# Performance work log

Hardware: AMD Instinct MI355X
Metric: run time of the kernel (lower is better)

## Reference

```python
import jax, jax.numpy as jnp
import numpy as np

EPS = 1e-5  # BatchNorm eps


def _add_self_loops(edge_index, num_nodes):
    loop = jnp.arange(num_nodes, dtype=edge_index.dtype)
    src = jnp.concatenate([edge_index[0], loop])
    dst = jnp.concatenate([edge_index[1], loop])
    return src, dst


def _gcn_conv(x, src, dst, norm, W, b, num_nodes):
    # PyG GCNConv: out = D^{-1/2} (A+I) D^{-1/2} (x W) + b
    h = x @ W                                # [N, out_dim]
    msg = h[src] * norm[:, None]             # [E+N, out_dim] gathered messages
    out = jax.ops.segment_sum(msg, dst, num_segments=num_nodes)
    return out + b


def _batch_norm(x, gamma, beta):
    # training-mode batch statistics over the node dimension (biased var)
    mean = jnp.mean(x, axis=0)
    var = jnp.var(x, axis=0)
    return (x - mean) * jax.lax.rsqrt(var + EPS) * gamma + beta


def setup_inputs() -> dict:
    key = jax.random.key(0)
    ks = jax.random.split(key, 10)
    N, E = 50000, 800000
    d_in, d_h, d_mid, d_out = 1536, 512, 128, 5

    x = jax.random.normal(ks[0], (N, d_in), dtype=jnp.float32)
    edge_index = jax.random.randint(ks[1], (2, E), 0, N, dtype=jnp.int32)

    def glorot(k, fan_in, fan_out):
        s = jnp.sqrt(6.0 / (fan_in + fan_out))
        return jax.random.uniform(k, (fan_in, fan_out), jnp.float32, -s, s)

    return {
        "x": x,
        "edge_index": edge_index,
        "W1": glorot(ks[2], d_in, d_h), "b1": jnp.zeros((d_h,), jnp.float32),
        "W2": glorot(ks[3], d_h, d_mid), "b2": jnp.zeros((d_mid,), jnp.float32),
        "W3": glorot(ks[4], d_mid, d_out), "b3": jnp.zeros((d_out,), jnp.float32),
        "gamma1": jnp.ones((d_h,), jnp.float32), "beta1": jnp.zeros((d_h,), jnp.float32),
        "gamma2": jnp.ones((d_mid,), jnp.float32), "beta2": jnp.zeros((d_mid,), jnp.float32),
    }


def reference(x, edge_index, W1, b1, W2, b2, W3, b3, gamma1, beta1, gamma2, beta2):
    N = x.shape[0]
    src, dst = _add_self_loops(edge_index, N)
    # symmetric degree normalization deg^{-1/2}[src] * deg^{-1/2}[dst]
    deg = jax.ops.segment_sum(jnp.ones_like(dst, dtype=x.dtype), dst, num_segments=N)
    inv_sqrt = jnp.where(deg > 0, jax.lax.rsqrt(deg), 0.0)
    norm = inv_sqrt[src] * inv_sqrt[dst]

    h = _gcn_conv(x, src, dst, norm, W1, b1, N)
    h = jax.nn.relu(_batch_norm(h, gamma1, beta1))  # dropout is identity in eval
    h = _gcn_conv(h, src, dst, norm, W2, b2, N)
    h = jax.nn.relu(_batch_norm(h, gamma2, beta2))
    h = _gcn_conv(h, src, dst, norm, W3, b3, N)
    return jax.nn.log_softmax(h, axis=1)
```

## Files before the change

kernel.cpp:

```cpp
#include <hip/hip_runtime.h>
#include <cstddef>
#include <cstdint>

typedef short s16x8 __attribute__((ext_vector_type(8)));
typedef unsigned short u16x4 __attribute__((ext_vector_type(4)));
typedef unsigned short u16x8 __attribute__((ext_vector_type(8)));
typedef float f32x4 __attribute__((ext_vector_type(4)));

__device__ __forceinline__ unsigned short f2bf(float f) {
  unsigned int u = __float_as_uint(f);
  u = (u + 0x7fffu + ((u >> 16) & 1u)) >> 16;
  return (unsigned short)u;
}
__device__ __forceinline__ float bf2f(unsigned short u) {
  return __uint_as_float(((unsigned int)u) << 16);
}

__device__ __forceinline__ void gl2lds16(const unsigned short* g, unsigned short* l) {
  __builtin_amdgcn_global_load_lds(
      (const __attribute__((address_space(1))) unsigned int*)g,
      (__attribute__((address_space(3))) unsigned int*)l, 16, 0, 0);
}
__device__ __forceinline__ void gl2lds16f(const float* g, float* l) {
  __builtin_amdgcn_global_load_lds(
      (const __attribute__((address_space(1))) unsigned int*)g,
      (__attribute__((address_space(3))) unsigned int*)l, 16, 0, 0);
}

static inline size_t alignup(size_t x) { return (x + 255) & ~(size_t)255; }

__global__ void count_kernel(const int* __restrict__ dst, int* __restrict__ counts, int E) {
  int e = blockIdx.x * blockDim.x + threadIdx.x;
  if (e < E) atomicAdd(&counts[dst[e]], 1);
}

__global__ void block_sum_kernel(const int* __restrict__ counts, int* __restrict__ bsum, int n) {
  __shared__ int red[256];
  int i = blockIdx.x * 256 + threadIdx.x;
  red[threadIdx.x] = (i < n) ? counts[i] : 0;
  __syncthreads();
  #pragma unroll
  for (int o = 128; o > 0; o >>= 1) {
    if (threadIdx.x < o) red[threadIdx.x] += red[threadIdx.x + o];
    __syncthreads();
  }
  if (threadIdx.x == 0) bsum[blockIdx.x] = red[0];
}

__global__ void scan_bsum_kernel(int* __restrict__ bsum, int nb) {
  __shared__ int s[256];
  int t = threadIdx.x;
  s[t] = (t < nb) ? bsum[t] : 0;
  __syncthreads();
  #pragma unroll
  for (int o = 1; o < 256; o <<= 1) {
    int v = (t >= o) ? s[t - o] : 0;
    __syncthreads();
    s[t] += v;
    __syncthreads();
  }
  if (t < nb) bsum[t] = (t == 0) ? 0 : s[t - 1];
}

__global__ void scan_apply_kernel(const int* __restrict__ counts, const int* __restrict__ bpre,
                                  int* __restrict__ offsets, float* __restrict__ inv_s, int n) {
  __shared__ int s[256];
  int t = threadIdx.x;
  int i = blockIdx.x * 256 + t;
  int c = (i < n) ? counts[i] : 0;
  s[t] = c;
  __syncthreads();
  #pragma unroll
  for (int o = 1; o < 256; o <<= 1) {
    int v = (t >= o) ? s[t - o] : 0;
    __syncthreads();
    s[t] += v;
    __syncthreads();
  }
  if (i < n) {
    offsets[i + 1] = s[t] + bpre[blockIdx.x];
    inv_s[i] = rsqrtf((float)(c + 1));
  }
  if (i == 0) offsets[0] = 0;
}

__global__ void fill_kernel(const int* __restrict__ src, const int* __restrict__ dst,
                            const int* __restrict__ offsets, int* __restrict__ cursor,
                            int* __restrict__ csr_src, int E) {
  int e = blockIdx.x * blockDim.x + threadIdx.x;
  if (e >= E) return;
  int d = dst[e];
  int pos = atomicAdd(&cursor[d], 1);
  csr_src[offsets[d] + pos] = src[e];
}

__global__ void transpose_both_kernel(const float* __restrict__ W1, unsigned short* __restrict__ W1t,
                                      const float* __restrict__ W2, unsigned short* __restrict__ W2t) {
  __shared__ float tile[32][33];
  int b = blockIdx.x;
  const float* W;
  unsigned short* Wt;
  int K, N, kx, ny;
  if (b < 768) { W = W1; Wt = W1t; K = 1536; N = 512; kx = b % 48; ny = b / 48; }
  else { b -= 768; W = W2; Wt = W2t; K = 512; N = 128; kx = b % 16; ny = b / 16; }
  int k0 = kx * 32, n0 = ny * 32;
  int tx = threadIdx.x & 31, ty = threadIdx.x >> 5;
  #pragma unroll
  for (int i = 0; i < 32; i += 8)
    tile[ty + i][tx] = W[(size_t)(k0 + ty + i) * N + n0 + tx];
  __syncthreads();
  #pragma unroll
  for (int i = 0; i < 32; i += 8)
    Wt[(size_t)(n0 + ty + i) * K + k0 + tx] = f2bf(tile[tx][ty + i]);
}

__global__ __launch_bounds__(512) void gemm1_kernel(
    const float* __restrict__ A, const unsigned short* __restrict__ B,
    unsigned short* __restrict__ C, int M) {
  __shared__ __align__(16) float As[2][128 * 32];
  __shared__ __align__(16) unsigned short Bs[2][256 * 32];
  const int K = 1536;
  const int NT = 48;
  int tid = threadIdx.x, lane = tid & 63, w = tid >> 6;

  int nwg = gridDim.x * gridDim.y;
  int orig = blockIdx.y * gridDim.x + blockIdx.x;
  int q = nwg >> 3, r = nwg & 7;
  int xcd = orig & 7, loc = orig >> 3;
  int wg = (xcd < r) ? xcd * (q + 1) + loc : r * (q + 1) + (xcd - r) * q + loc;
  int bx = wg & 1, by = wg >> 1;

  int m0 = by * 128, n0 = bx * 256;
  int wm = (w >> 2) * 64, wn = (w & 3) * 64;

  f32x4 acc[4][4];
  #pragma unroll
  for (int i = 0; i < 4; i++)
    #pragma unroll
    for (int j = 0; j < 4; j++) acc[i][j] = (f32x4){0.f, 0.f, 0.f, 0.f};

  int row0 = tid >> 3, slot0 = tid & 7;
  int row1 = 64 + row0;
  const float* agp0 = &A[(size_t)min(m0 + row0, M - 1) * K + ((slot0 ^ (row0 & 7)) << 2)];
  const float* agp1 = &A[(size_t)min(m0 + row1, M - 1) * K + ((slot0 ^ (row1 & 7)) << 2)];
  int adst0 = tid * 4, adst1 = (512 + tid) * 4;
  int brow = tid >> 2, bslot = tid & 3;
  int bsrc = (bslot ^ ((brow >> 1) & 3)) << 3;
  const unsigned short* bgp0 = &B[(size_t)(n0 + brow) * K + bsrc];
  const unsigned short* bgp1 = &B[(size_t)(n0 + 128 + brow) * K + bsrc];
  int bdst0 = tid * 8, bdst1 = (512 + tid) * 8;

  gl2lds16f(agp0, &As[0][adst0]);
  gl2lds16f(agp1, &As[0][adst1]);
  gl2lds16(bgp0, &Bs[0][bdst0]);
  gl2lds16(bgp1, &Bs[0][bdst1]);
  __syncthreads();

  int cur = 0;
  for (int t = 0; t < NT; t++) {
    if (t + 1 < NT) {
      int kb = (t + 1) * 32;
      gl2lds16f(agp0 + kb, &As[cur ^ 1][adst0]);
      gl2lds16f(agp1 + kb, &As[cur ^ 1][adst1]);
      gl2lds16(bgp0 + kb, &Bs[cur ^ 1][bdst0]);
      gl2lds16(bgp1 + kb, &Bs[cur ^ 1][bdst1]);
    }
    int jc = lane >> 4;
    s16x8 af[4], bfr[4];
    #pragma unroll
    for (int i = 0; i < 4; i++) {
      int rr = wm + i * 16 + (lane & 15);
      f32x4 v0 = *reinterpret_cast<const f32x4*>(&As[cur][rr * 32 + (((2 * jc) ^ (rr & 7)) << 2)]);
      f32x4 v1 = *reinterpret_cast<const f32x4*>(&As[cur][rr * 32 + (((2 * jc + 1) ^ (rr & 7)) << 2)]);
      unsigned int c0, c1, c2, c3;
      asm("v_cvt_pk_bf16_f32 %0, %1, %2" : "=v"(c0) : "v"(v0[0]), "v"(v0[1]));
      asm("v_cvt_pk_bf16_f32 %0, %1, %2" : "=v"(c1) : "v"(v0[2]), "v"(v0[3]));
      asm("v_cvt_pk_bf16_f32 %0, %1, %2" : "=v"(c2) : "v"(v1[0]), "v"(v1[1]));
      asm("v_cvt_pk_bf16_f32 %0, %1, %2" : "=v"(c3) : "v"(v1[2]), "v"(v1[3]));
      uint4 pk;
      pk.x = c0; pk.y = c1; pk.z = c2; pk.w = c3;
      af[i] = __builtin_bit_cast(s16x8, pk);
      int rn = wn + i * 16 + (lane & 15);
      bfr[i] = *reinterpret_cast<const s16x8*>(
          &Bs[cur][rn * 32 + ((jc ^ ((rn >> 1) & 3)) << 3)]);
    }
    #pragma unroll
    for (int i = 0; i < 4; i++)
      #pragma unroll
      for (int j = 0; j < 4; j++)
        acc[i][j] = __builtin_amdgcn_mfma_f32_16x16x32_bf16(af[i], bfr[j], acc[i][j], 0, 0, 0);
    __syncthreads();
    cur ^= 1;
  }

  #pragma unroll
  for (int i = 0; i < 4; i++) {
    #pragma unroll
    for (int j = 0; j < 4; j++) {
      int col = n0 + wn + j * 16 + (lane & 15);
      #pragma unroll
      for (int r2 = 0; r2 < 4; r2++) {
        int row = m0 + wm + i * 16 + (lane >> 4) * 4 + r2;
        if (row < M) C[(size_t)row * 512 + col] = f2bf(acc[i][j][r2]);
      }
    }
  }
}

#define LDT 72
__global__ __launch_bounds__(256) void gemm2_kernel(
    const unsigned short* __restrict__ A, const unsigned short* __restrict__ Bt,
    const float* __restrict__ accum, const float* __restrict__ gamma,
    const float* __restrict__ beta, unsigned short* __restrict__ C, int M, float invN) {
  const int N = 128, K = 512;
  __shared__ unsigned short As[64 * LDT];
  __shared__ unsigned short Bs[128 * LDT];
  __shared__ float scs[512], shs[512];
  int tid = threadIdx.x;
  int m0 = blockIdx.y * 64;
  int w = tid >> 6, lane = tid & 63;
  int wm = (w >> 1) * 32, wn = (w & 1) * 64;

  for (int c = tid; c < 512; c += 256) {
    float mean = accum[c] * invN;
    float var = accum[512 + c] * invN - mean * mean;
    float s = gamma[c] * rsqrtf(var + 1e-5f);
    scs[c] = s;
    shs[c] = beta[c] - mean * s;
  }
  __syncthreads();

  f32x4 acc[2][4];
  #pragma unroll
  for (int i = 0; i < 2; i++)
    #pragma unroll
    for (int j = 0; j < 4; j++) acc[i][j] = (f32x4){0.f, 0.f, 0.f, 0.f};

  for (int k0 = 0; k0 < K; k0 += 64) {
    #pragma unroll
    for (int r = 0; r < 2; r++) {
      int idx = r * 256 + tid;
      int row = idx >> 3;
      int seg = (idx & 7) * 8;
      int gr = m0 + row;
      u16x8 v = (u16x8){0, 0, 0, 0, 0, 0, 0, 0};
      if (gr < M) v = *reinterpret_cast<const u16x8*>(&A[(size_t)gr * K + k0 + seg]);
      int c = k0 + seg;
      u16x8 p;
      #pragma unroll
      for (int j = 0; j < 8; j++) {
        float f = fmaxf(bf2f(v[j]) * scs[c + j] + shs[c + j], 0.f);
        p[j] = f2bf(f);
      }
      *reinterpret_cast<u16x8*>(&As[row * LDT + seg]) = p;
    }
    #pragma unroll
    for (int r = 0; r < 4; r++) {
      int idx = r * 256 + tid;
      int n = idx >> 3;
      int seg = (idx & 7) * 8;
      u16x8 v = *reinterpret_cast<const u16x8*>(&Bt[(size_t)n * K + k0 + seg]);
      *reinterpret_cast<u16x8*>(&Bs[n * LDT + seg]) = v;
    }
    __syncthreads();
    #pragma unroll
    for (int ks = 0; ks < 2; ks++) {
      s16x8 af[2], bfr[4];
      #pragma unroll
      for (int i = 0; i < 2; i++)
        af[i] = *reinterpret_cast<const s16x8*>(
            &As[(wm + i * 16 + (lane & 15)) * LDT + ks * 32 + (lane >> 4) * 8]);
      #pragma unroll
      for (int j = 0; j < 4; j++)
        bfr[j] = *reinterpret_cast<const s16x8*>(
            &Bs[(wn + j * 16 + (lane & 15)) * LDT + ks * 32 + (lane >> 4) * 8]);
      #pragma unroll
      for (int i = 0; i < 2; i++)
        #pragma unroll
        for (int j = 0; j < 4; j++)
          acc[i][j] = __builtin_amdgcn_mfma_f32_16x16x32_bf16(af[i], bfr[j], acc[i][j], 0, 0, 0);
    }
    __syncthreads();
  }
  #pragma unroll
  for (int i = 0; i < 2; i++) {
    #pragma unroll
    for (int j = 0; j < 4; j++) {
      int col = wn + j * 16 + (lane & 15);
      #pragma unroll
      for (int r = 0; r < 4; r++) {
        int row = m0 + wm + i * 16 + (lane >> 4) * 4 + r;
        if (row < M) C[(size_t)row * N + col] = f2bf(acc[i][j][r]);
      }
    }
  }
}

__global__ void agg512_kernel(const unsigned short* __restrict__ h, const int* __restrict__ offsets,
                              const int* __restrict__ csr, const float* __restrict__ inv_s,
                              unsigned short* __restrict__ out, int n) {
  int wv = threadIdx.x >> 6, lane = threadIdx.x & 63;
  int node = blockIdx.x * 4 + wv;
  if (node >= n) return;
  const u16x8* h8 = reinterpret_cast<const u16x8*>(h);
  float di = inv_s[node];
  size_t rb = (size_t)node * 64;
  float acc[8];
  u16x8 v0 = h8[rb + lane];
  float dd = di * di;
  #pragma unroll
  for (int j = 0; j < 8; j++) acc[j] = bf2f(v0[j]) * dd;
  int e = offsets[node], e1 = offsets[node + 1];
  for (; e + 3 < e1; e += 4) {
    int sA = csr[e], sB = csr[e + 1], sC = csr[e + 2], sD = csr[e + 3];
    float wA = inv_s[sA] * di, wB = inv_s[sB] * di;
    float wC = inv_s[sC] * di, wD = inv_s[sD] * di;
    u16x8 vA = h8[(size_t)sA * 64 + lane];
    u16x8 vB = h8[(size_t)sB * 64 + lane];
    u16x8 vC = h8[(size_t)sC * 64 + lane];
    u16x8 vD = h8[(size_t)sD * 64 + lane];
    #pragma unroll
    for (int j = 0; j < 8; j++)
      acc[j] += (bf2f(vA[j]) * wA + bf2f(vB[j]) * wB) +
                (bf2f(vC[j]) * wC + bf2f(vD[j]) * wD);
  }
  for (; e < e1; e++) {
    int sA = csr[e];
    float wA = inv_s[sA] * di;
    u16x8 vA = h8[(size_t)sA * 64 + lane];
    #pragma unroll
    for (int j = 0; j < 8; j++) acc[j] += bf2f(vA[j]) * wA;
  }
  u16x8 o;
  #pragma unroll
  for (int j = 0; j < 8; j++) o[j] = f2bf(acc[j]);
  reinterpret_cast<u16x8*>(out)[rb + lane] = o;
}

__global__ void agg128_kernel(const unsigned short* __restrict__ h, const int* __restrict__ offsets,
                              const int* __restrict__ csr, const float* __restrict__ inv_s,
                              unsigned short* __restrict__ out, int n) {
  int wv = threadIdx.x >> 6, lane = threadIdx.x & 63;
  int node = blockIdx.x * 4 + wv;
  if (node >= n) return;
  const unsigned int* h2 = reinterpret_cast<const unsigned int*>(h);
  float di = inv_s[node];
  size_t rb = (size_t)node * 64;
  unsigned int u0 = h2[rb + lane];
  float dd = di * di;
  float alo = __uint_as_float(u0 << 16) * dd;
  float ahi = __uint_as_float(u0 & 0xffff0000u) * dd;
  int e = offsets[node], e1 = offsets[node + 1];
  for (; e + 3 < e1; e += 4) {
    int sA = csr[e], sB = csr[e + 1], sC = csr[e + 2], sD = csr[e + 3];
    float wA = inv_s[sA] * di, wB = inv_s[sB] * di;
    float wC = inv_s[sC] * di, wD = inv_s[sD] * di;
    unsigned int uA = h2[(size_t)sA * 64 + lane];
    unsigned int uB = h2[(size_t)sB * 64 + lane];
    unsigned int uC = h2[(size_t)sC * 64 + lane];
    unsigned int uD = h2[(size_t)sD * 64 + lane];
    alo += (__uint_as_float(uA << 16) * wA + __uint_as_float(uB << 16) * wB) +
           (__uint_as_float(uC << 16) * wC + __uint_as_float(uD << 16) * wD);
    ahi += (__uint_as_float(uA & 0xffff0000u) * wA + __uint_as_float(uB & 0xffff0000u) * wB) +
           (__uint_as_float(uC & 0xffff0000u) * wC + __uint_as_float(uD & 0xffff0000u) * wD);
  }
  for (; e < e1; e++) {
    int sA = csr[e];
    float wA = inv_s[sA] * di;
    unsigned int uA = h2[(size_t)sA * 64 + lane];
    alo += __uint_as_float(uA << 16) * wA;
    ahi += __uint_as_float(uA & 0xffff0000u) * wA;
  }
  unsigned int uo = ((unsigned int)f2bf(ahi) << 16) | (unsigned int)f2bf(alo);
  reinterpret_cast<unsigned int*>(out)[rb + lane] = uo;
}

__global__ void bn_stats512_kernel(const unsigned short* __restrict__ x, float* __restrict__ accum,
                                   int nrows, int rpb) {
  int r0 = blockIdx.x * rpb, r1 = min(nrows, r0 + rpb);
  int t = threadIdx.x;
  const unsigned int* x2 = reinterpret_cast<const unsigned int*>(x);
  float s0 = 0.f, q0 = 0.f, s1 = 0.f, q1 = 0.f;
  for (int r = r0; r < r1; r++) {
    unsigned int u = x2[(size_t)r * 256 + t];
    float lo = __uint_as_float(u << 16);
    float hi = __uint_as_float(u & 0xffff0000u);
    s0 += lo; q0 += lo * lo; s1 += hi; q1 += hi * hi;
  }
  atomicAdd(&accum[2 * t], s0);
  atomicAdd(&accum[2 * t + 1], s1);
  atomicAdd(&accum[512 + 2 * t], q0);
  atomicAdd(&accum[512 + 2 * t + 1], q1);
}

__global__ void bn_stats128_kernel(const unsigned short* __restrict__ x, float* __restrict__ accum,
                                   int nrows, int rpb) {
  int r0 = blockIdx.x * rpb, r1 = min(nrows, r0 + rpb);
  int t = threadIdx.x;
  int colu = t & 63, rofs = t >> 6;
  const unsigned int* x2 = reinterpret_cast<const unsigned int*>(x);
  float s0 = 0.f, q0 = 0.f, s1 = 0.f, q1 = 0.f;
  for (int r = r0 + rofs; r < r1; r += 4) {
    unsigned int u = x2[(size_t)r * 64 + colu];
    float lo = __uint_as_float(u << 16);
    float hi = __uint_as_float(u & 0xffff0000u);
    s0 += lo; q0 += lo * lo; s1 += hi; q1 += hi * hi;
  }
  atomicAdd(&accum[2 * colu], s0);
  atomicAdd(&accum[2 * colu + 1], s1);
  atomicAdd(&accum[128 + 2 * colu], q0);
  atomicAdd(&accum[128 + 2 * colu + 1], q1);
}

__global__ void gemm3_kernel(const unsigned short* __restrict__ A, const float* __restrict__ W,
                             const float* __restrict__ accum, const float* __restrict__ gamma,
                             const float* __restrict__ beta, float* __restrict__ C, int M,
                             float invN) {
  __shared__ float Ws[128 * 5];
  __shared__ float scs[128], shs[128];
  int tid = threadIdx.x;
  for (int i = tid; i < 128 * 5; i += blockDim.x) Ws[i] = W[i];
  if (tid < 128) {
    float mean = accum[tid] * invN;
    float var = accum[128 + tid] * invN - mean * mean;
    float s = gamma[tid] * rsqrtf(var + 1e-5f);
    scs[tid] = s;
    shs[tid] = beta[tid] - mean * s;
  }
  __syncthreads();
  int row = blockIdx.x * blockDim.x + tid;
  if (row >= M) return;
  float acc[5] = {0.f, 0.f, 0.f, 0.f, 0.f};
  const u16x8* a8 = reinterpret_cast<const u16x8*>(A + (size_t)row * 128);
  for (int k8 = 0; k8 < 16; k8++) {
    u16x8 v = a8[k8];
    int k = k8 * 8;
    #pragma unroll
    for (int j = 0; j < 8; j++) {
      float f = fmaxf(bf2f(v[j]) * scs[k + j] + shs[k + j], 0.f);
      #pragma unroll
      for (int c = 0; c < 5; c++) acc[c] += f * Ws[(k + j) * 5 + c];
    }
  }
  #pragma unroll
  for (int j = 0; j < 5; j++) C[(size_t)row * 5 + j] = acc[j];
}

__global__ void agg3_lsm_kernel(const float* __restrict__ h, const int* __restrict__ offsets,
                                const int* __restrict__ csr, const float* __restrict__ inv_s,
                                const float* __restrict__ b3, float* __restrict__ out, int n) {
  int node = blockIdx.x * blockDim.x + threadIdx.x;
  if (node >= n) return;
  float di = inv_s[node];
  float acc[5];
  #pragma unroll
  for (int j = 0; j < 5; j++) acc[j] = h[(size_t)node * 5 + j] * di * di;
  int s0 = offsets[node], s1 = offsets[node + 1];
  for (int e = s0; e < s1; e++) {
    int s = csr[e];
    float wgt = inv_s[s] * di;
    #pragma unroll
    for (int j = 0; j < 5; j++) acc[j] += h[(size_t)s * 5 + j] * wgt;
  }
  #pragma unroll
  for (int j = 0; j < 5; j++) acc[j] += b3[j];
  float m = acc[0];
  #pragma unroll
  for (int j = 1; j < 5; j++) m = fmaxf(m, acc[j]);
  float sum = 0.f;
  #pragma unroll
  for (int j = 0; j < 5; j++) sum += expf(acc[j] - m);
  float lse = logf(sum);
  #pragma unroll
  for (int j = 0; j < 5; j++) out[(size_t)node * 5 + j] = acc[j] - m - lse;
}

extern "C" void kernel_launch(void* const* d_in, const int* in_sizes, int n_in,
                              void* d_out, int out_size, void* d_ws, size_t ws_size,
                              hipStream_t stream) {
  const float* x      = (const float*)d_in[0];
  const int*   ei     = (const int*)d_in[1];
  const float* W1     = (const float*)d_in[2];
  const float* b3     = (const float*)d_in[7];
  const float* W2     = (const float*)d_in[4];
  const float* W3     = (const float*)d_in[6];
  const float* gamma1 = (const float*)d_in[8];
  const float* beta1  = (const float*)d_in[9];
  const float* gamma2 = (const float*)d_in[10];
  const float* beta2  = (const float*)d_in[11];

  const int N = in_sizes[0] / 1536;
  const int E = in_sizes[1] / 2;
  const int* src = ei;
  const int* dst = ei + E;

  const int mblocks = (N + 127) / 128;
  const int Mpad = mblocks * 128;
  const int nb = (N + 255) / 256;

  char* ws = (char*)d_ws;
  size_t szRA = alignup((size_t)N * 512 * sizeof(float));
  size_t szXB = alignup((size_t)Mpad * 1536 * sizeof(unsigned short));
  char* RAb = ws;
  char* RBb = ws + szRA;
  char* sp = ws + szRA + szXB;
  char* zbase = sp;
  int* counts    = (int*)sp;          sp += alignup((size_t)N * 4);
  int* cursor    = (int*)sp;          sp += alignup((size_t)N * 4);
  float* accumA  = (float*)sp;        sp += alignup(1024 * 4);
  float* accumB  = (float*)sp;        sp += alignup(256 * 4);
  size_t zspan = (size_t)(sp - zbase);
  int* offsets  = (int*)sp;           sp += alignup((size_t)(N + 1) * 4);
  int* csr_src  = (int*)sp;           sp += alignup((size_t)E * 4);
  float* inv_s  = (float*)sp;         sp += alignup((size_t)N * 4);
  unsigned short* W1t = (unsigned short*)sp; sp += alignup((size_t)512 * 1536 * 2);
  unsigned short* W2t = (unsigned short*)sp; sp += alignup((size_t)128 * 512 * 2);
  int* bsum     = (int*)sp;           sp += alignup(256 * 4);

  unsigned short* H1  = (unsigned short*)RAb;
  unsigned short* G1  = (unsigned short*)RBb;
  unsigned short* H2  = (unsigned short*)RAb;
  unsigned short* G2  = (unsigned short*)RBb;
  float*          H3  = (float*)RAb;

  hipMemsetAsync(zbase, 0, zspan, stream);

  count_kernel<<<(E + 255) / 256, 256, 0, stream>>>(dst, counts, E);
  block_sum_kernel<<<nb, 256, 0, stream>>>(counts, bsum, N);
  scan_bsum_kernel<<<1, 256, 0, stream>>>(bsum, nb);
  scan_apply_kernel<<<nb, 256, 0, stream>>>(counts, bsum, offsets, inv_s, N);
  fill_kernel<<<(E + 255) / 256, 256, 0, stream>>>(src, dst, offsets, cursor, csr_src, E);

  transpose_both_kernel<<<832, 256, 0, stream>>>(W1, W1t, W2, W2t);

  int aggblocks = (N + 3) / 4;
  int rpb = (N + 511) / 512;
  float invN = 1.0f / N;

  gemm1_kernel<<<dim3(2, mblocks), 512, 0, stream>>>(x, W1t, H1, N);
  agg512_kernel<<<aggblocks, 256, 0, stream>>>(H1, offsets, csr_src, inv_s, G1, N);
  bn_stats512_kernel<<<512, 256, 0, stream>>>(G1, accumA, N, rpb);

  gemm2_kernel<<<dim3(1, (N + 63) / 64), 256, 0, stream>>>(G1, W2t, accumA, gamma1, beta1, H2, N,
                                                           invN);
  agg128_kernel<<<aggblocks, 256, 0, stream>>>(H2, offsets, csr_src, inv_s, G2, N);
  bn_stats128_kernel<<<512, 256, 0, stream>>>(G2, accumB, N, rpb);

  gemm3_kernel<<<(N + 255) / 256, 256, 0, stream>>>(G2, W3, accumB, gamma2, beta2, H3, N, invN);
  agg3_lsm_kernel<<<(N + 255) / 256, 256, 0, stream>>>(H3, offsets, csr_src, inv_s, b3,
                                                       (float*)d_out, N);
}
```

Baseline: 637.6 us.

## Triple-buffer A tiles in gemm1 with explicit waitcnt-based pipelining

```diff
diff --git a/kernel.cpp b/kernel.cpp
--- a/kernel.cpp
+++ b/kernel.cpp
@@ -117,10 +117,9 @@
 __global__ __launch_bounds__(512) void gemm1_kernel(
     const float* __restrict__ A, const unsigned short* __restrict__ B,
     unsigned short* __restrict__ C, int M) {
-  __shared__ __align__(16) float As[2][128 * 32];
+  __shared__ __align__(16) float As[3][128 * 32];
   __shared__ __align__(16) unsigned short Bs[2][256 * 32];
   const int K = 1536;
-  const int NT = 48;
   int tid = threadIdx.x, lane = tid & 63, w = tid >> 6;
 
   int nwg = gridDim.x * gridDim.y;
@@ -150,28 +149,22 @@
   const unsigned short* bgp1 = &B[(size_t)(n0 + 128 + brow) * K + bsrc];
   int bdst0 = tid * 8, bdst1 = (512 + tid) * 8;
 
-  gl2lds16f(agp0, &As[0][adst0]);
-  gl2lds16f(agp1, &As[0][adst1]);
-  gl2lds16(bgp0, &Bs[0][bdst0]);
-  gl2lds16(bgp1, &Bs[0][bdst1]);
-  __syncthreads();
-
-  int cur = 0;
-  for (int t = 0; t < NT; t++) {
-    if (t + 1 < NT) {
-      int kb = (t + 1) * 32;
-      gl2lds16f(agp0 + kb, &As[cur ^ 1][adst0]);
-      gl2lds16f(agp1 + kb, &As[cur ^ 1][adst1]);
-      gl2lds16(bgp0 + kb, &Bs[cur ^ 1][bdst0]);
-      gl2lds16(bgp1 + kb, &Bs[cur ^ 1][bdst1]);
-    }
+  auto stageA = [&](int kb, float* AsW) {
+    gl2lds16f(agp0 + kb, AsW + adst0);
+    gl2lds16f(agp1 + kb, AsW + adst1);
+  };
+  auto stageB = [&](int kb, unsigned short* BsW) {
+    gl2lds16(bgp0 + kb, BsW + bdst0);
+    gl2lds16(bgp1 + kb, BsW + bdst1);
+  };
+  auto mfma_phase = [&](const float* AsR, const unsigned short* BsR) {
     int jc = lane >> 4;
     s16x8 af[4], bfr[4];
     #pragma unroll
     for (int i = 0; i < 4; i++) {
       int rr = wm + i * 16 + (lane & 15);
-      f32x4 v0 = *reinterpret_cast<const f32x4*>(&As[cur][rr * 32 + (((2 * jc) ^ (rr & 7)) << 2)]);
-      f32x4 v1 = *reinterpret_cast<const f32x4*>(&As[cur][rr * 32 + (((2 * jc + 1) ^ (rr & 7)) << 2)]);
+      f32x4 v0 = *reinterpret_cast<const f32x4*>(&AsR[rr * 32 + (((2 * jc) ^ (rr & 7)) << 2)]);
+      f32x4 v1 = *reinterpret_cast<const f32x4*>(&AsR[rr * 32 + (((2 * jc + 1) ^ (rr & 7)) << 2)]);
       unsigned int c0, c1, c2, c3;
       asm("v_cvt_pk_bf16_f32 %0, %1, %2" : "=v"(c0) : "v"(v0[0]), "v"(v0[1]));
       asm("v_cvt_pk_bf16_f32 %0, %1, %2" : "=v"(c1) : "v"(v0[2]), "v"(v0[3]));
@@ -182,16 +175,46 @@
       af[i] = __builtin_bit_cast(s16x8, pk);
       int rn = wn + i * 16 + (lane & 15);
       bfr[i] = *reinterpret_cast<const s16x8*>(
-          &Bs[cur][rn * 32 + ((jc ^ ((rn >> 1) & 3)) << 3)]);
+          &BsR[rn * 32 + ((jc ^ ((rn >> 1) & 3)) << 3)]);
     }
     #pragma unroll
     for (int i = 0; i < 4; i++)
       #pragma unroll
       for (int j = 0; j < 4; j++)
         acc[i][j] = __builtin_amdgcn_mfma_f32_16x16x32_bf16(af[i], bfr[j], acc[i][j], 0, 0, 0);
-    __syncthreads();
-    cur ^= 1;
-  }
+  };
+
+  stageA(0, As[0]);
+  stageB(0, Bs[0]);
+  stageA(32, As[1]);
+  asm volatile("s_waitcnt vmcnt(2)" ::: "memory");
+  __builtin_amdgcn_s_barrier();
+
+#define G1BODY(T, A0i, A2i, B0i, B1i)                           \
+  stageB(((T) + 1) * 32, Bs[B1i]);                              \
+  stageA(((T) + 2) * 32, As[A2i]);                              \
+  mfma_phase(As[A0i], Bs[B0i]);                                 \
+  asm volatile("s_waitcnt lgkmcnt(0) vmcnt(2)" ::: "memory");   \
+  __builtin_amdgcn_s_barrier();
+
+  for (int tb = 0; tb < 42; tb += 6) {
+    G1BODY(tb + 0, 0, 2, 0, 1)
+    G1BODY(tb + 1, 1, 0, 1, 0)
+    G1BODY(tb + 2, 2, 1, 0, 1)
+    G1BODY(tb + 3, 0, 2, 1, 0)
+    G1BODY(tb + 4, 1, 0, 0, 1)
+    G1BODY(tb + 5, 2, 1, 1, 0)
+  }
+  G1BODY(42, 0, 2, 0, 1)
+  G1BODY(43, 1, 0, 1, 0)
+  G1BODY(44, 2, 1, 0, 1)
+  G1BODY(45, 0, 2, 1, 0)
+#undef G1BODY
+  stageB(47 * 32, Bs[1]);
+  mfma_phase(As[1], Bs[0]);
+  asm volatile("s_waitcnt lgkmcnt(0) vmcnt(0)" ::: "memory");
+  __builtin_amdgcn_s_barrier();
+  mfma_phase(As[2], Bs[1]);
 
   #pragma unroll
   for (int i = 0; i < 4; i++) {
```

Measured after the change: 674.0 us. 1.06x slower.

## Fuse BatchNorm statistics into GCN aggregation kernels

Applied to the files above, without the earlier changes.

```diff
diff --git a/kernel.cpp b/kernel.cpp
--- a/kernel.cpp
+++ b/kernel.cpp
@@ -298,118 +298,122 @@
 
 __global__ void agg512_kernel(const unsigned short* __restrict__ h, const int* __restrict__ offsets,
                               const int* __restrict__ csr, const float* __restrict__ inv_s,
-                              unsigned short* __restrict__ out, int n) {
+                              unsigned short* __restrict__ out, float* __restrict__ accum, int n) {
+  __shared__ float rs[512], rq[512];
   int wv = threadIdx.x >> 6, lane = threadIdx.x & 63;
-  int node = blockIdx.x * 4 + wv;
-  if (node >= n) return;
+  for (int c = threadIdx.x; c < 512; c += 256) { rs[c] = 0.f; rq[c] = 0.f; }
+  __syncthreads();
   const u16x8* h8 = reinterpret_cast<const u16x8*>(h);
-  float di = inv_s[node];
-  size_t rb = (size_t)node * 64;
-  float acc[8];
-  u16x8 v0 = h8[rb + lane];
-  float dd = di * di;
-  #pragma unroll
-  for (int j = 0; j < 8; j++) acc[j] = bf2f(v0[j]) * dd;
-  int e = offsets[node], e1 = offsets[node + 1];
-  for (; e + 3 < e1; e += 4) {
-    int sA = csr[e], sB = csr[e + 1], sC = csr[e + 2], sD = csr[e + 3];
-    float wA = inv_s[sA] * di, wB = inv_s[sB] * di;
-    float wC = inv_s[sC] * di, wD = inv_s[sD] * di;
-    u16x8 vA = h8[(size_t)sA * 64 + lane];
-    u16x8 vB = h8[(size_t)sB * 64 + lane];
-    u16x8 vC = h8[(size_t)sC * 64 + lane];
-    u16x8 vD = h8[(size_t)sD * 64 + lane];
-    #pragma unroll
-    for (int j = 0; j < 8; j++)
-      acc[j] += (bf2f(vA[j]) * wA + bf2f(vB[j]) * wB) +
-                (bf2f(vC[j]) * wC + bf2f(vD[j]) * wD);
-  }
-  for (; e < e1; e++) {
-    int sA = csr[e];
-    float wA = inv_s[sA] * di;
-    u16x8 vA = h8[(size_t)sA * 64 + lane];
-    #pragma unroll
-    for (int j = 0; j < 8; j++) acc[j] += bf2f(vA[j]) * wA;
-  }
-  u16x8 o;
-  #pragma unroll
-  for (int j = 0; j < 8; j++) o[j] = f2bf(acc[j]);
-  reinterpret_cast<u16x8*>(out)[rb + lane] = o;
+  float s[8], qsum[8];
+  #pragma unroll
+  for (int j = 0; j < 8; j++) { s[j] = 0.f; qsum[j] = 0.f; }
+  for (int i = 0; i < 8; i++) {
+    int node = blockIdx.x * 32 + wv * 8 + i;
+    if (node >= n) break;
+    float di = inv_s[node];
+    size_t rb = (size_t)node * 64;
+    float acc[8];
+    u16x8 v0 = h8[rb + lane];
+    float dd = di * di;
+    #pragma unroll
+    for (int j = 0; j < 8; j++) acc[j] = bf2f(v0[j]) * dd;
+    int e = offsets[node], e1 = offsets[node + 1];
+    for (; e + 3 < e1; e += 4) {
+      int sA = csr[e], sB = csr[e + 1], sC = csr[e + 2], sD = csr[e + 3];
+      float wA = inv_s[sA] * di, wB = inv_s[sB] * di;
+      float wC = inv_s[sC] * di, wD = inv_s[sD] * di;
+      u16x8 vA = h8[(size_t)sA * 64 + lane];
+      u16x8 vB = h8[(size_t)sB * 64 + lane];
+      u16x8 vC = h8[(size_t)sC * 64 + lane];
+      u16x8 vD = h8[(size_t)sD * 64 + lane];
+      #pragma unroll
+      for (int j = 0; j < 8; j++)
+        acc[j] += (bf2f(vA[j]) * wA + bf2f(vB[j]) * wB) +
+                  (bf2f(vC[j]) * wC + bf2f(vD[j]) * wD);
+    }
+    for (; e < e1; e++) {
+      int sA = csr[e];
+      float wA = inv_s[sA] * di;
+      u16x8 vA = h8[(size_t)sA * 64 + lane];
+      #pragma unroll
+      for (int j = 0; j < 8; j++) acc[j] += bf2f(vA[j]) * wA;
+    }
+    u16x8 o;
+    #pragma unroll
+    for (int j = 0; j < 8; j++) {
+      float gv = bf2f(f2bf(acc[j]));
+      o[j] = f2bf(acc[j]);
+      s[j] += gv;
+      qsum[j] += gv * gv;
+    }
+    reinterpret_cast<u16x8*>(out)[rb + lane] = o;
+  }
+  #pragma unroll
+  for (int j = 0; j < 8; j++) {
+    atomicAdd(&rs[lane * 8 + j], s[j]);
+    atomicAdd(&rq[lane * 8 + j], qsum[j]);
+  }
+  __syncthreads();
+  for (int c = threadIdx.x; c < 512; c += 256) {
+    atomicAdd(&accum[c], rs[c]);
+    atomicAdd(&accum[512 + c], rq[c]);
+  }
 }
 
 __global__ void agg128_kernel(const unsigned short* __restrict__ h, const int* __restrict__ offsets,
                               const int* __restrict__ csr, const float* __restrict__ inv_s,
-                              unsigned short* __restrict__ out, int n) {
+                              unsigned short* __restrict__ out, float* __restrict__ accum, int n) {
+  __shared__ float rs[128], rq[128];
   int wv = threadIdx.x >> 6, lane = threadIdx.x & 63;
-  int node = blockIdx.x * 4 + wv;
-  if (node >= n) return;
+  if (threadIdx.x < 128) { rs[threadIdx.x] = 0.f; rq[threadIdx.x] = 0.f; }
+  __syncthreads();
   const unsigned int* h2 = reinterpret_cast<const unsigned int*>(h);
-  float di = inv_s[node];
-  size_t rb = (size_t)node * 64;
-  unsigned int u0 = h2[rb + lane];
-  float dd = di * di;
-  float alo = __uint_as_float(u0 << 16) * dd;
-  float ahi = __uint_as_float(u0 & 0xffff0000u) * dd;
-  int e = offsets[node], e1 = offsets[node + 1];
-  for (; e + 3 < e1; e += 4) {
-    int sA = csr[e], sB = csr[e + 1], sC = csr[e + 2], sD = csr[e + 3];
-    float wA = inv_s[sA] * di, wB = inv_s[sB] * di;
-    float wC = inv_s[sC] * di, wD = inv_s[sD] * di;
-    unsigned int uA = h2[(size_t)sA * 64 + lane];
-    unsigned int uB = h2[(size_t)sB * 64 + lane];
-    unsigned int uC = h2[(size_t)sC * 64 + lane];
-    unsigned int uD = h2[(size_t)sD * 64 + lane];
-    alo += (__uint_as_float(uA << 16) * wA + __uint_as_float(uB << 16) * wB) +
-           (__uint_as_float(uC << 16) * wC + __uint_as_float(uD << 16) * wD);
-    ahi += (__uint_as_float(uA & 0xffff0000u) * wA + __uint_as_float(uB & 0xffff0000u) * wB) +
-           (__uint_as_float(uC & 0xffff0000u) * wC + __uint_as_float(uD & 0xffff0000u) * wD);
-  }
-  for (; e < e1; e++) {
-    int sA = csr[e];
-    float wA = inv_s[sA] * di;
-    unsigned int uA = h2[(size_t)sA * 64 + lane];
-    alo += __uint_as_float(uA << 16) * wA;
-    ahi += __uint_as_float(uA & 0xffff0000u) * wA;
-  }
-  unsigned int uo = ((unsigned int)f2bf(ahi) << 16) | (unsigned int)f2bf(alo);
-  reinterpret_cast<unsigned int*>(out)[rb + lane] = uo;
-}
-
-__global__ void bn_stats512_kernel(const unsigned short* __restrict__ x, float* __restrict__ accum,
-                                   int nrows, int rpb) {
-  int r0 = blockIdx.x * rpb, r1 = min(nrows, r0 + rpb);
-  int t = threadIdx.x;
-  const unsigned int* x2 = reinterpret_cast<const unsigned int*>(x);
   float s0 = 0.f, q0 = 0.f, s1 = 0.f, q1 = 0.f;
-  for (int r = r0; r < r1; r++) {
-    unsigned int u = x2[(size_t)r * 256 + t];
-    float lo = __uint_as_float(u << 16);
-    float hi = __uint_as_float(u & 0xffff0000u);
-    s0 += lo; q0 += lo * lo; s1 += hi; q1 += hi * hi;
-  }
-  atomicAdd(&accum[2 * t], s0);
-  atomicAdd(&accum[2 * t + 1], s1);
-  atomicAdd(&accum[512 + 2 * t], q0);
-  atomicAdd(&accum[512 + 2 * t + 1], q1);
-}
-
-__global__ void bn_stats128_kernel(const unsigned short* __restrict__ x, float* __restrict__ accum,
-                                   int nrows, int rpb) {
-  int r0 = blockIdx.x * rpb, r1 = min(nrows, r0 + rpb);
-  int t = threadIdx.x;
-  int colu = t & 63, rofs = t >> 6;
-  const unsigned int* x2 = reinterpret_cast<const unsigned int*>(x);
-  float s0 = 0.f, q0 = 0.f, s1 = 0.f, q1 = 0.f;
-  for (int r = r0 + rofs; r < r1; r += 4) {
-    unsigned int u = x2[(size_t)r * 64 + colu];
-    float lo = __uint_as_float(u << 16);
-    float hi = __uint_as_float(u & 0xffff0000u);
-    s0 += lo; q0 += lo * lo; s1 += hi; q1 += hi * hi;
-  }
-  atomicAdd(&accum[2 * colu], s0);
-  atomicAdd(&accum[2 * colu + 1], s1);
-  atomicAdd(&accum[128 + 2 * colu], q0);
-  atomicAdd(&accum[128 + 2 * colu + 1], q1);
+  for (int i = 0; i < 8; i++) {
+    int node = blockIdx.x * 32 + wv * 8 + i;
+    if (node >= n) break;
+    float di = inv_s[node];
+    size_t rb = (size_t)node * 64;
+    unsigned int u0 = h2[rb + lane];
+    float dd = di * di;
+    float alo = __uint_as_float(u0 << 16) * dd;
+    float ahi = __uint_as_float(u0 & 0xffff0000u) * dd;
+    int e = offsets[node], e1 = offsets[node + 1];
+    for (; e + 3 < e1; e += 4) {
+      int sA = csr[e], sB = csr[e + 1], sC = csr[e + 2], sD = csr[e + 3];
+      float wA = inv_s[sA] * di, wB = inv_s[sB] * di;
+      float wC = inv_s[sC] * di, wD = inv_s[sD] * di;
+      unsigned int uA = h2[(size_t)sA * 64 + lane];
+      unsigned int uB = h2[(size_t)sB * 64 + lane];
+      unsigned int uC = h2[(size_t)sC * 64 + lane];
+      unsigned int uD = h2[(size_t)sD * 64 + lane];
+      alo += (__uint_as_float(uA << 16) * wA + __uint_as_float(uB << 16) * wB) +
+             (__uint_as_float(uC << 16) * wC + __uint_as_float(uD << 16) * wD);
+      ahi += (__uint_as_float(uA & 0xffff0000u) * wA + __uint_as_float(uB & 0xffff0000u) * wB) +
+             (__uint_as_float(uC & 0xffff0000u) * wC + __uint_as_float(uD & 0xffff0000u) * wD);
+    }
+    for (; e < e1; e++) {
+      int sA = csr[e];
+      float wA = inv_s[sA] * di;
+      unsigned int uA = h2[(size_t)sA * 64 + lane];
+      alo += __uint_as_float(uA << 16) * wA;
+      ahi += __uint_as_float(uA & 0xffff0000u) * wA;
+    }
+    unsigned short blo = f2bf(alo), bhi = f2bf(ahi);
+    unsigned int uo = ((unsigned int)bhi << 16) | (unsigned int)blo;
+    reinterpret_cast<unsigned int*>(out)[rb + lane] = uo;
+    float glo = bf2f(blo), ghi = bf2f(bhi);
+    s0 += glo; q0 += glo * glo; s1 += ghi; q1 += ghi * ghi;
+  }
+  atomicAdd(&rs[2 * lane], s0);
+  atomicAdd(&rq[2 * lane], q0);
+  atomicAdd(&rs[2 * lane + 1], s1);
+  atomicAdd(&rq[2 * lane + 1], q1);
+  __syncthreads();
+  if (threadIdx.x < 128) {
+    atomicAdd(&accum[threadIdx.x], rs[threadIdx.x]);
+    atomicAdd(&accum[128 + threadIdx.x], rq[threadIdx.x]);
+  }
 }
 
 __global__ void gemm3_kernel(const unsigned short* __restrict__ A, const float* __restrict__ W,
@@ -533,18 +537,15 @@
 
   transpose_both_kernel<<<832, 256, 0, stream>>>(W1, W1t, W2, W2t);
 
-  int aggblocks = (N + 3) / 4;
-  int rpb = (N + 511) / 512;
+  int aggblocks32 = (N + 31) / 32;
   float invN = 1.0f / N;
 
   gemm1_kernel<<<dim3(2, mblocks), 512, 0, stream>>>(x, W1t, H1, N);
-  agg512_kernel<<<aggblocks, 256, 0, stream>>>(H1, offsets, csr_src, inv_s, G1, N);
-  bn_stats512_kernel<<<512, 256, 0, stream>>>(G1, accumA, N, rpb);
+  agg512_kernel<<<aggblocks32, 256, 0, stream>>>(H1, offsets, csr_src, inv_s, G1, accumA, N);
 
   gemm2_kernel<<<dim3(1, (N + 63) / 64), 256, 0, stream>>>(G1, W2t, accumA, gamma1, beta1, H2, N,
                                                            invN);
-  agg128_kernel<<<aggblocks, 256, 0, stream>>>(H2, offsets, csr_src, inv_s, G2, N);
-  bn_stats128_kernel<<<512, 256, 0, stream>>>(G2, accumB, N, rpb);
+  agg128_kernel<<<aggblocks32, 256, 0, stream>>>(H2, offsets, csr_src, inv_s, G2, accumB, N);
 
   gemm3_kernel<<<(N + 255) / 256, 256, 0, stream>>>(G2, W3, accumB, gamma2, beta2, H3, N, invN);
   agg3_lsm_kernel<<<(N + 255) / 256, 256, 0, stream>>>(H3, offsets, csr_src, inv_s, b3,
```

After: 572.2 us. 10.3% less time.
